# Kernel optimization log

Hardware: AMD Instinct MI355X
Metric: run time of the kernel (lower is better)

Reference implementation:

```python
import jax, jax.numpy as jnp
import numpy as np

DIM = 512
GLBL = 108
N = 100000
NUM_SEGMENTS = 1024


def setup_inputs() -> dict:
    key = jax.random.key(0)
    ks = jax.random.split(key, 9)
    x = jax.random.normal(ks[0], (N, DIM), dtype=jnp.float32)
    glbl_x = jax.random.normal(ks[1], (N, GLBL), dtype=jnp.float32)
    batch = jnp.sort(jax.random.randint(ks[2], (N,), 0, NUM_SEGMENTS, dtype=jnp.int32))
    # MLP params: (dim+108 -> dim), (dim -> dim), (dim -> 1)
    s0 = 1.0 / np.sqrt(DIM + GLBL)
    s1 = 1.0 / np.sqrt(DIM)
    W0 = jax.random.uniform(ks[3], (DIM + GLBL, DIM), jnp.float32, -s0, s0)
    b0 = jax.random.uniform(ks[4], (DIM,), jnp.float32, -s0, s0)
    W1 = jax.random.uniform(ks[5], (DIM, DIM), jnp.float32, -s1, s1)
    b1 = jax.random.uniform(ks[6], (DIM,), jnp.float32, -s1, s1)
    W2 = jax.random.uniform(ks[7], (DIM, 1), jnp.float32, -s1, s1)
    b2 = jax.random.uniform(ks[8], (1,), jnp.float32, -s1, s1)
    return {"x": x, "batch": batch, "glbl_x": glbl_x,
            "W0": W0, "b0": b0, "W1": W1, "b1": b1, "W2": W2, "b2": b2}


def segment_softmax(logits, seg, num_segments):
    # logits: [N, 1]; per-segment numerically-stable softmax (torch_geometric softmax)
    m = jax.ops.segment_max(logits, seg, num_segments=num_segments)  # [G, 1]
    e = jnp.exp(logits - m[seg])
    s = jax.ops.segment_sum(e, seg, num_segments=num_segments)       # [G, 1]
    return e / (s[seg] + 1e-16)


def reference(x, batch, glbl_x, W0, b0, W1, b1, W2, b2):
    out = jnp.concatenate([x, glbl_x], axis=-1)          # [N, dim+108]
    out = jax.nn.softplus(out @ W0 + b0)                 # [N, dim]
    out = jax.nn.softplus(out @ W1 + b1)                 # [N, dim]
    out = out @ W2 + b2                                  # [N, 1]
    return segment_softmax(out, batch, NUM_SEGMENTS)     # [N, 1]
```

## Files before the change

### kernel.cpp

```cpp
#include <hip/hip_runtime.h>
#include <hip/hip_bf16.h>
#include <math.h>


#define NSEG 1024

typedef __attribute__((ext_vector_type(8))) short short8;
typedef __attribute__((ext_vector_type(4))) float f32x4;

__device__ __forceinline__ unsigned short f2bf(float f) {
  __hip_bfloat16 h = __float2bfloat16(f);
  return *reinterpret_cast<unsigned short*>(&h);
}
__device__ __forceinline__ float softplus_fast(float z) {
  float t = __expf(-fabsf(z));
  return fmaxf(z, 0.f) + __logf(1.f + t);
}
__device__ __forceinline__ void gll16(const void* g, void* l) {
  __builtin_amdgcn_global_load_lds(
      (const __attribute__((address_space(1))) void*)g,
      (__attribute__((address_space(3))) void*)l, 16, 0, 0);
}
__device__ __forceinline__ int xcd_swz(int bid, int nwg) {
  int q = nwg >> 3, r = nwg & 7, x = bid & 7, i = bid >> 3;
  return (x < r ? x * (q + 1) : r * (q + 1) + (x - r) * q) + i;
}

__global__ __launch_bounds__(256) void prep(const float* __restrict__ W0,
                                            const float* __restrict__ W1,
                                            unsigned short* __restrict__ W0T,
                                            unsigned short* __restrict__ W1T,
                                            float* __restrict__ logits, int Mp) {
  int t = blockIdx.x * 256 + threadIdx.x;
  if (t < 512 * 640) {
    int n = t / 640, k = t % 640;
    W0T[t] = f2bf(k < 620 ? W0[(size_t)k * 512 + n] : 0.f);
    return;
  }
  t -= 512 * 640;
  if (t < 512 * 512) {
    int n = t / 512, k = t % 512;
    W1T[t] = f2bf(W1[(size_t)k * 512 + n]);
    return;
  }
  t -= 512 * 512;
  if (t < Mp) logits[t] = 0.f;
}

__global__ __launch_bounds__(256) void pack_g(const float* __restrict__ gx,
                                              float* __restrict__ G32,
                                              int N, int Mp) {
  int t = blockIdx.x * 256 + threadIdx.x;
  if (t >= Mp * 32) return;
  int row = t >> 5, c = (t & 31) << 2;
  float4 v;
  v.x = (row < N && c + 0 < 108) ? gx[(size_t)row * 108 + c + 0] : 0.f;
  v.y = (row < N && c + 1 < 108) ? gx[(size_t)row * 108 + c + 1] : 0.f;
  v.z = (row < N && c + 2 < 108) ? gx[(size_t)row * 108 + c + 2] : 0.f;
  v.w = (row < N && c + 3 < 108) ? gx[(size_t)row * 108 + c + 3] : 0.f;
  *reinterpret_cast<float4*>(G32 + (size_t)row * 128 + c) = v;
}

__global__ __launch_bounds__(256, 3) void gemm0(const float* __restrict__ x,
                                                const float* __restrict__ G32,
                                                const unsigned short* __restrict__ W0T,
                                                const float* __restrict__ b0,
                                                unsigned short* __restrict__ H0,
                                                int N, int nwg) {
  constexpr int K = 640, KT = 20;
  __shared__ float Asf[2][128 * 32];
  __shared__ unsigned short Ws[2][128 * 32];
  const int L = xcd_swz(blockIdx.x, nwg);
  const int nt = L & 3, mt = L >> 2;
  const int tid = threadIdx.x, lane = tid & 63, wid = tid >> 6;
  const int wm = wid >> 1, wn = wid & 1, lm = lane & 15, rch = lane >> 4;

  const unsigned short* Wg = W0T + (size_t)(nt * 128) * K;

  f32x4 acc[4][4] = {};

  auto stageA = [&](int buf, int kb) {
#pragma unroll
    for (int i2 = 0; i2 < 4; ++i2) {
      int f = i2 * 256 + tid;
      int rb = f >> 7, pl = (f >> 6) & 1, rr = (f >> 2) & 15, cs = f & 3;
      int r = rb * 16 + rr;
      int g = 2 * (cs ^ ((rr >> 1) & 3)) + pl;
      int col = kb + g * 4;
      const float* src;
      if (kb < 512) {
        int rg = mt * 128 + r; if (rg >= N) rg = N - 1;
        src = x + (size_t)rg * 512 + col;
      } else {
        int rg = mt * 128 + r;
        src = G32 + (size_t)rg * 128 + (col - 512);
      }
      gll16(src, &Asf[buf][f * 4]);
    }
  };
  auto stageW = [&](int buf, int kb) {
#pragma unroll
    for (int i2 = 0; i2 < 2; ++i2) {
      int f = i2 * 256 + tid;
      int row = f >> 2;
      int sc = ((f & 3) ^ ((row >> 1) & 3)) << 3;
      gll16(Wg + (size_t)row * K + kb + sc, &Ws[buf][f * 8]);
    }
  };

  stageA(0, 0);
  stageW(0, 0);

  for (int kt = 0; kt < KT; ++kt) {
    const int cur = kt & 1;
    __syncthreads();
    if (kt + 1 < KT) { stageA(cur ^ 1, (kt + 1) * 32); stageW(cur ^ 1, (kt + 1) * 32); }

    const int cs = rch ^ ((lm >> 1) & 3);
    short8 af[4], wf[4];
#pragma unroll
    for (int mi = 0; mi < 4; ++mi) {
      const int rb = wm * 4 + mi;
      const float* base = &Asf[cur][rb * 512 + lm * 16 + cs * 4];
      f32x4 lo = *reinterpret_cast<const f32x4*>(base);
      f32x4 hi = *reinterpret_cast<const f32x4*>(base + 256);
      union { unsigned short u[8]; short8 s8; } cv;
#pragma unroll
      for (int j = 0; j < 4; ++j) { cv.u[j] = f2bf(lo[j]); cv.u[4 + j] = f2bf(hi[j]); }
      af[mi] = cv.s8;
    }
#pragma unroll
    for (int ni = 0; ni < 4; ++ni) {
      int rw = wn * 64 + ni * 16 + lm;
      wf[ni] = *reinterpret_cast<const short8*>(
          &Ws[cur][rw * 32 + ((rch ^ ((rw >> 1) & 3)) << 3)]);
    }
    __builtin_amdgcn_s_setprio(1);
#pragma unroll
    for (int mi = 0; mi < 4; ++mi)
#pragma unroll
      for (int ni = 0; ni < 4; ++ni)
        acc[mi][ni] = __builtin_amdgcn_mfma_f32_16x16x32_bf16(wf[ni], af[mi], acc[mi][ni], 0, 0, 0);
    __builtin_amdgcn_s_setprio(0);
  }

#pragma unroll
  for (int mi = 0; mi < 4; ++mi) {
    const int m = mt * 128 + wm * 64 + mi * 16 + lm;
#pragma unroll
    for (int ni = 0; ni < 4; ++ni) {
      const int n0 = nt * 128 + wn * 64 + ni * 16 + (rch << 2);
      const f32x4 bb = *reinterpret_cast<const f32x4*>(b0 + n0);
      f32x4 v = acc[mi][ni];
      union { unsigned short u[4]; uint2 qv; } o;
#pragma unroll
      for (int rr = 0; rr < 4; ++rr) o.u[rr] = f2bf(softplus_fast(v[rr] + bb[rr]));
      *reinterpret_cast<uint2*>(H0 + (size_t)m * 512 + n0) = o.qv;
    }
  }
}

__global__ __launch_bounds__(256, 4) void gemm1(const unsigned short* __restrict__ H0,
                                                const unsigned short* __restrict__ W1T,
                                                const float* __restrict__ b1,
                                                const float* __restrict__ W2,
                                                float* __restrict__ logits, int nwg) {
  constexpr int K = 512, KT = 16;
  __shared__ unsigned short As[2][128 * 32];
  __shared__ unsigned short Ws[2][128 * 32];
  const int L = xcd_swz(blockIdx.x, nwg);
  const int nt = L & 3, mt = L >> 2;
  const int tid = threadIdx.x, lane = tid & 63, wid = tid >> 6;
  const int wm = wid >> 1, wn = wid & 1, lm = lane & 15, rch = lane >> 4;

  const unsigned short* Ag = H0 + (size_t)(mt * 128) * K;
  const unsigned short* Wg = W1T + (size_t)(nt * 128) * K;

  f32x4 acc[4][4] = {};

  auto stage = [&](int buf, int kb) {
#pragma unroll
    for (int i2 = 0; i2 < 2; ++i2) {
      int f = i2 * 256 + tid;
      int row = f >> 2;
      int sc = ((f & 3) ^ ((row >> 1) & 3)) << 3;
      gll16(Ag + (size_t)row * K + kb + sc, &As[buf][f * 8]);
      gll16(Wg + (size_t)row * K + kb + sc, &Ws[buf][f * 8]);
    }
  };

  stage(0, 0);

  for (int kt = 0; kt < KT; ++kt) {
    const int cur = kt & 1;
    __syncthreads();
    if (kt + 1 < KT) stage(cur ^ 1, (kt + 1) * 32);

    short8 af[4], wf[4];
#pragma unroll
    for (int mi = 0; mi < 4; ++mi) {
      int rw = wm * 64 + mi * 16 + lm;
      af[mi] = *reinterpret_cast<const short8*>(
          &As[cur][rw * 32 + ((rch ^ ((rw >> 1) & 3)) << 3)]);
    }
#pragma unroll
    for (int ni = 0; ni < 4; ++ni) {
      int rw = wn * 64 + ni * 16 + lm;
      wf[ni] = *reinterpret_cast<const short8*>(
          &Ws[cur][rw * 32 + ((rch ^ ((rw >> 1) & 3)) << 3)]);
    }
    __builtin_amdgcn_s_setprio(1);
#pragma unroll
    for (int mi = 0; mi < 4; ++mi)
#pragma unroll
      for (int ni = 0; ni < 4; ++ni)
        acc[mi][ni] = __builtin_amdgcn_mfma_f32_16x16x32_bf16(wf[ni], af[mi], acc[mi][ni], 0, 0, 0);
    __builtin_amdgcn_s_setprio(0);
  }

#pragma unroll
  for (int mi = 0; mi < 4; ++mi) {
    const int m = mt * 128 + wm * 64 + mi * 16 + lm;
    float part = 0.f;
#pragma unroll
    for (int ni = 0; ni < 4; ++ni) {
      const int n0 = nt * 128 + wn * 64 + ni * 16 + (rch << 2);
      const f32x4 bb = *reinterpret_cast<const f32x4*>(b1 + n0);
      const f32x4 wv = *reinterpret_cast<const f32x4*>(W2 + n0);
      f32x4 v = acc[mi][ni];
#pragma unroll
      for (int rr = 0; rr < 4; ++rr) part += softplus_fast(v[rr] + bb[rr]) * wv[rr];
    }
    part += __shfl_xor(part, 16);
    part += __shfl_xor(part, 32);
    if (lane < 16) atomicAdd(logits + m, part);
  }
}

__global__ __launch_bounds__(256) void segsoftmax(const float* __restrict__ logits,
                                                  const int* __restrict__ batch,
                                                  float* __restrict__ out, int N) {
  const int g = blockIdx.x;
  const int tid = threadIdx.x;
  int lo = 0, hi = N;
  while (lo < hi) { int mid = (lo + hi) >> 1; if (batch[mid] < g) lo = mid + 1; else hi = mid; }
  const int beg = lo;
  hi = N;
  while (lo < hi) { int mid = (lo + hi) >> 1; if (batch[mid] < g + 1) lo = mid + 1; else hi = mid; }
  const int end = lo;
  if (beg >= end) return;

  __shared__ float sh[4];
  float m = -INFINITY;
  for (int i = beg + tid; i < end; i += 256) m = fmaxf(m, logits[i]);
#pragma unroll
  for (int o = 32; o; o >>= 1) m = fmaxf(m, __shfl_down(m, o));
  if ((tid & 63) == 0) sh[tid >> 6] = m;
  __syncthreads();
  m = fmaxf(fmaxf(sh[0], sh[1]), fmaxf(sh[2], sh[3]));
  __syncthreads();

  float s = 0.f;
  for (int i = beg + tid; i < end; i += 256) s += expf(logits[i] - m);
#pragma unroll
  for (int o = 32; o; o >>= 1) s += __shfl_down(s, o);
  if ((tid & 63) == 0) sh[tid >> 6] = s;
  __syncthreads();
  s = sh[0] + sh[1] + sh[2] + sh[3];

  const float inv = 1.f / (s + 1e-16f);
  for (int i = beg + tid; i < end; i += 256) out[i] = expf(logits[i] - m) * inv;
}

extern "C" void kernel_launch(void* const* d_in, const int* in_sizes, int n_in,
                              void* d_out, int out_size, void* d_ws, size_t ws_size,
                              hipStream_t stream) {
  const float* x = (const float*)d_in[0];
  const int* batch = (const int*)d_in[1];
  const float* gx = (const float*)d_in[2];
  const float* W0 = (const float*)d_in[3];
  const float* b0 = (const float*)d_in[4];
  const float* W1 = (const float*)d_in[5];
  const float* b1 = (const float*)d_in[6];
  const float* W2 = (const float*)d_in[7];
  float* out = (float*)d_out;

  const int N = in_sizes[1];
  const int Mp = ((N + 127) / 128) * 128;
  const int nwg = (Mp / 128) * 4;

  auto align256 = [](size_t v) { return (v + 255) & ~(size_t)255; };
  char* ws = (char*)d_ws;
  size_t off = 0;
  float* G32 = (float*)(ws + off);                   off = align256(off + (size_t)Mp * 128 * 4);
  unsigned short* W0T = (unsigned short*)(ws + off); off = align256(off + (size_t)512 * 640 * 2);
  unsigned short* W1T = (unsigned short*)(ws + off); off = align256(off + (size_t)512 * 512 * 2);
  unsigned short* H0 = (unsigned short*)(ws + off);  off = align256(off + (size_t)Mp * 512 * 2);
  float* logits = (float*)(ws + off);                off = align256(off + (size_t)Mp * 4);
  (void)ws_size; (void)n_in; (void)out_size;

  const int prep_elems = 512 * 640 + 512 * 512 + Mp;
  prep<<<(prep_elems + 255) / 256, 256, 0, stream>>>(W0, W1, W0T, W1T, logits, Mp);
  pack_g<<<(Mp * 32 + 255) / 256, 256, 0, stream>>>(gx, G32, N, Mp);

  gemm0<<<nwg, 256, 0, stream>>>(x, G32, W0T, b0, H0, N, nwg);
  gemm1<<<nwg, 256, 0, stream>>>(H0, W1T, b1, W2, logits, nwg);

  segsoftmax<<<NSEG, 256, 0, stream>>>(logits, batch, out, N);
}
```

Baseline: 278.6 us.

## Pipeline gemm0 and gemm1 across M-chunks in a combined role-split kernel

Merges the two GEMM kernels into one launch that assigns each workgroup either the first-layer or second-layer role. Rows are split into four chunks and launched as five staggered kernels, so gemm0 on chunk k runs alongside gemm1 on chunk k-1. The goal is to fill the device with a mix of the two GEMMs and reduce the tail and idle time of two big sequential launches. The cost is more launches, a shared 48KB LDS allocation for both roles (which may lower occupancy for the gemm1 role), and launch bounds of 3 for both.

```diff
diff --git a/kernel.cpp b/kernel.cpp
--- a/kernel.cpp
+++ b/kernel.cpp
@@ -61,17 +61,17 @@
   *reinterpret_cast<float4*>(G32 + (size_t)row * 128 + c) = v;
 }
 
-__global__ __launch_bounds__(256, 3) void gemm0(const float* __restrict__ x,
-                                                const float* __restrict__ G32,
-                                                const unsigned short* __restrict__ W0T,
-                                                const float* __restrict__ b0,
-                                                unsigned short* __restrict__ H0,
-                                                int N, int nwg) {
+__device__ __forceinline__ void gemm0_body(char* lds, const float* __restrict__ x,
+                                           const float* __restrict__ G32,
+                                           const unsigned short* __restrict__ W0T,
+                                           const float* __restrict__ b0,
+                                           unsigned short* __restrict__ H0,
+                                           int N, int idx, int nwg, int mtb) {
   constexpr int K = 640, KT = 20;
-  __shared__ float Asf[2][128 * 32];
-  __shared__ unsigned short Ws[2][128 * 32];
-  const int L = xcd_swz(blockIdx.x, nwg);
-  const int nt = L & 3, mt = L >> 2;
+  float* Asf = (float*)lds;
+  unsigned short* Ws = (unsigned short*)(lds + 32768);
+  const int L = xcd_swz(idx, nwg);
+  const int nt = L & 3, mt = mtb + (L >> 2);
   const int tid = threadIdx.x, lane = tid & 63, wid = tid >> 6;
   const int wm = wid >> 1, wn = wid & 1, lm = lane & 15, rch = lane >> 4;
 
@@ -95,7 +95,7 @@
         int rg = mt * 128 + r;
         src = G32 + (size_t)rg * 128 + (col - 512);
       }
-      gll16(src, &Asf[buf][f * 4]);
+      gll16(src, &Asf[buf * 4096 + f * 4]);
     }
   };
   auto stageW = [&](int buf, int kb) {
@@ -104,7 +104,7 @@
       int f = i2 * 256 + tid;
       int row = f >> 2;
       int sc = ((f & 3) ^ ((row >> 1) & 3)) << 3;
-      gll16(Wg + (size_t)row * K + kb + sc, &Ws[buf][f * 8]);
+      gll16(Wg + (size_t)row * K + kb + sc, &Ws[buf * 4096 + f * 8]);
     }
   };
 
@@ -121,7 +121,7 @@
 #pragma unroll
     for (int mi = 0; mi < 4; ++mi) {
       const int rb = wm * 4 + mi;
-      const float* base = &Asf[cur][rb * 512 + lm * 16 + cs * 4];
+      const float* base = &Asf[cur * 4096 + rb * 512 + lm * 16 + cs * 4];
       f32x4 lo = *reinterpret_cast<const f32x4*>(base);
       f32x4 hi = *reinterpret_cast<const f32x4*>(base + 256);
       union { unsigned short u[8]; short8 s8; } cv;
@@ -133,7 +133,7 @@
     for (int ni = 0; ni < 4; ++ni) {
       int rw = wn * 64 + ni * 16 + lm;
       wf[ni] = *reinterpret_cast<const short8*>(
-          &Ws[cur][rw * 32 + ((rch ^ ((rw >> 1) & 3)) << 3)]);
+          &Ws[cur * 4096 + rw * 32 + ((rch ^ ((rw >> 1) & 3)) << 3)]);
     }
     __builtin_amdgcn_s_setprio(1);
 #pragma unroll
@@ -160,16 +160,18 @@
   }
 }
 
-__global__ __launch_bounds__(256, 4) void gemm1(const unsigned short* __restrict__ H0,
-                                                const unsigned short* __restrict__ W1T,
-                                                const float* __restrict__ b1,
-                                                const float* __restrict__ W2,
-                                                float* __restrict__ logits, int nwg) {
+__device__ __forceinline__ void gemm1_body(char* lds,
+                                           const unsigned short* __restrict__ H0,
+                                           const unsigned short* __restrict__ W1T,
+                                           const float* __restrict__ b1,
+                                           const float* __restrict__ W2,
+                                           float* __restrict__ logits,
+                                           int idx, int nwg, int mtb) {
   constexpr int K = 512, KT = 16;
-  __shared__ unsigned short As[2][128 * 32];
-  __shared__ unsigned short Ws[2][128 * 32];
-  const int L = xcd_swz(blockIdx.x, nwg);
-  const int nt = L & 3, mt = L >> 2;
+  unsigned short* As = (unsigned short*)lds;
+  unsigned short* Ws = (unsigned short*)(lds + 16384);
+  const int L = xcd_swz(idx, nwg);
+  const int nt = L & 3, mt = mtb + (L >> 2);
   const int tid = threadIdx.x, lane = tid & 63, wid = tid >> 6;
   const int wm = wid >> 1, wn = wid & 1, lm = lane & 15, rch = lane >> 4;
 
@@ -184,8 +186,8 @@
       int f = i2 * 256 + tid;
       int row = f >> 2;
       int sc = ((f & 3) ^ ((row >> 1) & 3)) << 3;
-      gll16(Ag + (size_t)row * K + kb + sc, &As[buf][f * 8]);
-      gll16(Wg + (size_t)row * K + kb + sc, &Ws[buf][f * 8]);
+      gll16(Ag + (size_t)row * K + kb + sc, &As[buf * 4096 + f * 8]);
+      gll16(Wg + (size_t)row * K + kb + sc, &Ws[buf * 4096 + f * 8]);
     }
   };
 
@@ -201,13 +203,13 @@
     for (int mi = 0; mi < 4; ++mi) {
       int rw = wm * 64 + mi * 16 + lm;
       af[mi] = *reinterpret_cast<const short8*>(
-          &As[cur][rw * 32 + ((rch ^ ((rw >> 1) & 3)) << 3)]);
+          &As[cur * 4096 + rw * 32 + ((rch ^ ((rw >> 1) & 3)) << 3)]);
     }
 #pragma unroll
     for (int ni = 0; ni < 4; ++ni) {
       int rw = wn * 64 + ni * 16 + lm;
       wf[ni] = *reinterpret_cast<const short8*>(
-          &Ws[cur][rw * 32 + ((rch ^ ((rw >> 1) & 3)) << 3)]);
+          &Ws[cur * 4096 + rw * 32 + ((rch ^ ((rw >> 1) & 3)) << 3)]);
     }
     __builtin_amdgcn_s_setprio(1);
 #pragma unroll
@@ -235,6 +237,32 @@
     part += __shfl_xor(part, 32);
     if (lane < 16) atomicAdd(logits + m, part);
   }
+}
+
+__global__ __launch_bounds__(256, 3) void megapipe(const float* __restrict__ x,
+                                                   const float* __restrict__ G32,
+                                                   const unsigned short* __restrict__ W0T,
+                                                   const float* __restrict__ b0,
+                                                   unsigned short* __restrict__ H0,
+                                                   const unsigned short* __restrict__ W1T,
+                                                   const float* __restrict__ b1,
+                                                   const float* __restrict__ W2,
+                                                   float* __restrict__ logits,
+                                                   int N, int mtb0, int nwg0,
+                                                   int mtb1, int nwg1) {
+  __shared__ __align__(16) char lds[49152];
+  const int kG = blockIdx.x >> 3, o = blockIdx.x & 7;
+  const int g0 = nwg0 >> 3, g1 = nwg1 >> 3;
+  const int gm = (g0 < g1) ? g0 : g1;
+  int role, gidx;
+  if (kG < 2 * gm) { role = kG & 1; gidx = kG >> 1; }
+  else             { role = (g0 > g1) ? 0 : 1; gidx = gm + (kG - 2 * gm); }
+  const int idx = gidx * 8 + o;
+
+  if (role == 0)
+    gemm0_body(lds, x, G32, W0T, b0, H0, N, idx, nwg0, mtb0);
+  else
+    gemm1_body(lds, H0, W1T, b1, W2, logits, idx, nwg1, mtb1);
 }
 
 __global__ __launch_bounds__(256) void segsoftmax(const float* __restrict__ logits,
@@ -287,7 +315,7 @@
 
   const int N = in_sizes[1];
   const int Mp = ((N + 127) / 128) * 128;
-  const int nwg = (Mp / 128) * 4;
+  const int blocksM = Mp / 128;
 
   auto align256 = [](size_t v) { return (v + 255) & ~(size_t)255; };
   char* ws = (char*)d_ws;
@@ -303,8 +331,26 @@
   prep<<<(prep_elems + 255) / 256, 256, 0, stream>>>(W0, W1, W0T, W1T, logits, Mp);
   pack_g<<<(Mp * 32 + 255) / 256, 256, 0, stream>>>(gx, G32, N, Mp);
 
-  gemm0<<<nwg, 256, 0, stream>>>(x, G32, W0T, b0, H0, N, nwg);
-  gemm1<<<nwg, 256, 0, stream>>>(H0, W1T, b1, W2, logits, nwg);
+  const int NCHUNK = 4;
+  int mchunk[NCHUNK], mtb[NCHUNK];
+  {
+    int mb = (blocksM / NCHUNK) & ~1;
+    int acc = 0;
+    for (int c = 0; c < NCHUNK; ++c) {
+      mchunk[c] = (c == NCHUNK - 1) ? (blocksM - acc) : mb;
+      mtb[c] = acc;
+      acc += mchunk[c];
+    }
+  }
+
+  for (int k = 0; k <= NCHUNK; ++k) {
+    const int nwg0 = (k < NCHUNK) ? mchunk[k] * 4 : 0;
+    const int mb0 = (k < NCHUNK) ? mtb[k] : 0;
+    const int nwg1 = (k >= 1) ? mchunk[k - 1] * 4 : 0;
+    const int mb1 = (k >= 1) ? mtb[k - 1] : 0;
+    megapipe<<<nwg0 + nwg1, 256, 0, stream>>>(x, G32, W0T, b0, H0, W1T, b1, W2,
+                                              logits, N, mb0, nwg0, mb1, nwg1);
+  }
 
   segsoftmax<<<NSEG, 256, 0, stream>>>(logits, batch, out, N);
 }
```

Measured after the change: 332.1 us. 19.2% more time.
